# Kernel optimization log

Hardware: AMD Instinct MI355X
Metric: run time of the kernel (lower is better)

The kernel has to match this reference:

```python
import jax, jax.numpy as jnp
import numpy as np

N_NODES = 1000
N_EDGES = 8000
IN_FEATS = 64
HID = 128
RDIM = HID // 2  # UniversalReadout output dim
EPS = 1e-5


def _lrelu(v):
    return jax.nn.leaky_relu(v, 0.01)


def setup_inputs() -> dict:
    key = jax.random.key(0)
    ks = jax.random.split(key, 16)
    B = 128
    node_feats = jax.random.normal(ks[0], (B * N_NODES, IN_FEATS), jnp.float32)
    edge_weights = jax.random.uniform(ks[1], (B * N_EDGES,), jnp.float32)
    g_weights = jax.random.uniform(ks[2], (B * N_NODES,), jnp.float32)
    src = jax.random.randint(ks[3], (N_EDGES,), 0, N_NODES)
    dst = jax.random.randint(ks[4], (N_EDGES,), 0, N_NODES)
    # GraphConv weights (in, out), kaiming-ish scale
    W1 = jax.random.normal(ks[5], (IN_FEATS, HID), jnp.float32) / np.sqrt(IN_FEATS)
    W2 = jax.random.normal(ks[6], (HID, HID), jnp.float32) / np.sqrt(HID)
    W3 = jax.random.normal(ks[7], (HID, HID), jnp.float32) / np.sqrt(HID)
    suppl = jnp.ones((3, N_EDGES), jnp.float32)           # suppl_weights_conv1..3
    AR = jnp.ones((4, N_NODES), jnp.float32)              # AR1..AR4 weights
    gn_gamma = jnp.ones((3, HID), jnp.float32)
    gn_beta = jnp.zeros((3, HID), jnp.float32)
    gn_alpha = jnp.ones((3, HID), jnp.float32)            # GraphNorm mean-scale
    phi_W = jax.random.normal(ks[8], (3, HID, HID), jnp.float32) / np.sqrt(HID)
    phi_b = jnp.zeros((3, HID), jnp.float32)
    rho_W = jax.random.normal(ks[9], (3, HID, RDIM), jnp.float32) / np.sqrt(HID)
    rho_b = jnp.zeros((3, RDIM), jnp.float32)
    return dict(node_feats=node_feats, edge_weights=edge_weights, g_weights=g_weights,
                W1=W1, W2=W2, W3=W3, suppl=suppl, AR=AR,
                gn_gamma=gn_gamma, gn_beta=gn_beta, gn_alpha=gn_alpha,
                phi_W=phi_W, phi_b=phi_b, rho_W=rho_W, rho_b=rho_b,
                src=src, dst=dst)


def _forward(node_feats, edge_weights, g_weights, W1, W2, W3, suppl, AR,
             gn_gamma, gn_beta, gn_alpha, phi_W, phi_b, rho_W, rho_b, src, dst):
    B = node_feats.shape[0] // N_NODES
    x = node_feats.reshape(B, N_NODES, -1)        # (B, N, F)
    gw = g_weights.reshape(B, N_NODES)            # (B, N)
    ew = edge_weights.reshape(B, N_EDGES)         # (B, E)

    # structural degree normalization (norm='both'), shared topology
    deg_out = jnp.maximum(jnp.zeros((N_NODES,), x.dtype).at[src].add(1.0), 1.0)
    deg_in = jnp.maximum(jnp.zeros((N_NODES,), x.dtype).at[dst].add(1.0), 1.0)
    n_out = deg_out ** -0.5
    n_in = deg_in ** -0.5

    def gconv(h, W, ew_l):
        hs = h * n_out[None, :, None]
        msgs = hs[:, src, :] * ew_l[:, :, None]                       # (B, E, D)
        agg = jnp.zeros_like(hs).at[:, dst].add(msgs)                  # scatter-add
        return (agg * n_in[None, :, None]) @ W

    def gnorm(h, i):
        mean = h.mean(axis=1, keepdims=True)
        sub = h - gn_alpha[i] * mean
        var = (sub * sub).mean(axis=1, keepdims=True)
        return gn_gamma[i] * sub * jax.lax.rsqrt(var + EPS) + gn_beta[i]

    def uro(h, i):  # UniversalReadout (deep-sets): per-node MLP -> sum -> MLP
        z = _lrelu(h @ phi_W[i] + phi_b[i]).sum(axis=1)
        return _lrelu(z @ rho_W[i] + rho_b[i])

    def wmean(h, ar):  # dgl.mean_nodes with node weight: mean over nodes of w*x
        w = gw * ar[None, :]
        return (w[:, :, None] * h).mean(axis=1)

    pieces = [wmean(x, AR[0])]
    h = x
    Ws = (W1, W2, W3)
    for i in range(3):
        h = _lrelu(gnorm(gconv(h, Ws[i], ew * suppl[i][None, :]), i))
        pieces.append(uro(h, i))
        pieces.append(wmean(h, AR[i + 1]))
    return _lrelu(jnp.concatenate(pieces, axis=-1))


def reference(node_feats, edge_weights, g_weights, W1, W2, W3, suppl, AR,
              gn_gamma, gn_beta, gn_alpha, phi_W, phi_b, rho_W, rho_b, src, dst):
    return _forward(node_feats, edge_weights, g_weights, W1, W2, W3, suppl, AR,
                    gn_gamma, gn_beta, gn_alpha, phi_W, phi_b, rho_W, rho_b, src, dst)
```

## Files before the change

### kernel.cpp

```cpp
#include <hip/hip_runtime.h>
#include <cstddef>

#define NN 1000
#define NE 8000
#define FIN 64
#define DH 128
#define RD 64
#define FEPS 1e-5f

typedef short short8 __attribute__((ext_vector_type(8)));
typedef float f32x4 __attribute__((ext_vector_type(4)));

__device__ __forceinline__ float lrelu(float x){ return x > 0.f ? x : 0.01f*x; }

__device__ __forceinline__ unsigned short f2b(float x){
  union { float f; unsigned int u; } v; v.f = x;
  unsigned int r = (v.u + 0x7fffu + ((v.u >> 16) & 1u)) >> 16;
  return (unsigned short)r;
}
__device__ __forceinline__ float b2f(unsigned int lo16){
  union { unsigned int u; float f; } v; v.u = lo16 << 16; return v.f;
}
__device__ __forceinline__ unsigned int pack2(float a, float b){
  return (unsigned int)f2b(a) | ((unsigned int)f2b(b) << 16);
}


__global__ __launch_bounds__(1024) void k_topo(const int* __restrict__ src,
                       const int* __restrict__ dst,
                       float* nout, float* nin, int* rp,
                       int* csr_s, int* csr_e, int* csr_d){
  __shared__ int sdo[1024], sdi[1024], ssc[1024], sfill[1024];
  int t = threadIdx.x;
  sdo[t] = 0; sdi[t] = 0;
  __syncthreads();
  for (int e = t; e < NE; e += 1024){
    atomicAdd(&sdo[src[e]], 1);
    atomicAdd(&sdi[dst[e]], 1);
  }
  __syncthreads();
  int d = sdi[t];
  ssc[t] = d; __syncthreads();
  for (int off = 1; off < 1024; off <<= 1){
    int v = (t >= off) ? ssc[t-off] : 0;
    __syncthreads();
    ssc[t] += v;
    __syncthreads();
  }
  int myrp = ssc[t] - d;
  if (t < NN){
    rp[t] = myrp;
    nin[t]  = rsqrtf((float)max(sdi[t], 1));
    nout[t] = rsqrtf((float)max(sdo[t], 1));
  }
  if (t == NN-1) rp[NN] = ssc[t];
  sfill[t] = myrp;
  __syncthreads();
  for (int e = t; e < NE; e += 1024){
    int dn = dst[e];
    int pos = atomicAdd(&sfill[dn], 1);
    csr_s[pos] = src[e];
    csr_e[pos] = e;
    csr_d[pos] = dn;
  }
}


__global__ __launch_bounds__(256) void k_edge(const float* __restrict__ ew,
        const float* __restrict__ sup, const float* __restrict__ nout,
        const float* __restrict__ nin, const int* __restrict__ csr_s,
        const int* __restrict__ csr_e, const int* __restrict__ csr_d,
        int2* __restrict__ ecl, int B){
  int bid = blockIdx.x, t = threadIdx.x;
  int layer, b, q;
  if ((B & 7) == 0){
    int xcd = bid & 7, r = bid >> 3;
    int bsub = r/12, rem = r - bsub*12;
    layer = rem >> 2; q = rem & 3; b = bsub*8 + xcd;
  } else {
    layer = bid/(4*B);
    int rem = bid - layer*4*B;
    b = rem >> 2; q = rem & 3;
  }
  const float* ewb  = ew  + (size_t)b*NE;
  const float* supl = sup + (size_t)layer*NE;
  int2* o = ecl + ((size_t)layer*B + b)*NE;
  for (int k = q*2000 + t; k < q*2000 + 2000; k += 256){
    int e = csr_e[k]; int s = csr_s[k];
    float wv = ewb[e]*supl[e]*nout[s]*nin[csr_d[k]];
    int2 v; v.x = s; v.y = __float_as_int(wv);
    o[k] = v;
  }
}


__global__ __launch_bounds__(256) void k_misc(
        const float* __restrict__ W1, const float* __restrict__ W2,
        const float* __restrict__ W3, const float* __restrict__ phiW,
        unsigned short* __restrict__ wt,
        const float* __restrict__ x, unsigned short* __restrict__ xbf,
        const float* __restrict__ gw, const float* __restrict__ AR,
        float* __restrict__ out, int B){
  __shared__ float red[4][64];
  int bid = blockIdx.x, t = threadIdx.x;
  if (bid < 352){
    int i = bid*256 + t;
    if (i < 8192){
      int n = i >> 6, k = i & 63;
      wt[i] = f2b(W1[k*128 + n]);
    } else if (i < 24576){
      int j = i - 8192; int n = j >> 7, k = j & 127;
      wt[i] = f2b(W2[k*128 + n]);
    } else if (i < 40960){
      int j = i - 24576; int n = j >> 7, k = j & 127;
      wt[i] = f2b(W3[k*128 + n]);
    } else if (i < 90112){
      int j = i - 40960; int m = j >> 14; int jj = j & 16383;
      int n = jj >> 7, k = jj & 127;
      wt[i] = f2b(phiW[m*16384 + k*128 + n]);
    }
  } else {
    int wb = bid - 352;
    int b, q;
    if ((B & 7) == 0){
      int xcd = wb & 7, r = wb >> 3;
      int bsub = r >> 2; q = r & 3; b = bsub*8 + xcd;
    } else { b = wb >> 2; q = wb & 3; }
    int r = t >> 6, l = t & 63;
    float acc = 0.f;
    int v0 = q*250;
    for (int v = v0 + r; v < v0 + 250; v += 4){
      size_t idx = ((size_t)b*NN + v)*FIN + l;
      float xv = x[idx];
      xbf[idx] = f2b(xv);
      acc += gw[(size_t)b*NN + v]*AR[v]*xv;
    }
    red[r][l] = acc;
    __syncthreads();
    if (t < 64){
      float s = red[0][t]+red[1][t]+red[2][t]+red[3][t];
      atomicAdd(&out[(size_t)b*640 + t], s*(1.f/NN));
    }
  }
}


__global__ __launch_bounds__(256) void k_gathF(const unsigned short* __restrict__ xbf,
        const int2* __restrict__ ec, const int* __restrict__ rp,
        unsigned short* __restrict__ agg, int B){
  int bid = blockIdx.x;
  int b, chunk;
  if ((B & 7) == 0){
    int xcd = bid & 7, r = bid >> 3;
    int bsub = r/63; chunk = r - bsub*63; b = bsub*8 + xcd;
  } else { b = bid/63; chunk = bid - b*63; }
  int t = threadIdx.x;
  int grp = t >> 4, j = t & 15;
  int v = chunk*16 + grp; if (v >= NN) v = NN-1;
  int kb = rp[v], ke = rp[v+1];
  const unsigned short* xb = xbf + (size_t)b*NN*FIN;
  const int2* ecb = ec + (size_t)b*NE;
  float acc[4][4] = {};
  int k = kb;
  for (; k+3 < ke; k += 4){
    #pragma unroll
    for (int uu = 0; uu < 4; ++uu){
      int2 e = ecb[k+uu];
      uint2 u = *(const uint2*)(xb + e.x*FIN + j*4);
      float wgt = __int_as_float(e.y);
      acc[uu][0] = fmaf(b2f(u.x & 0xffffu), wgt, acc[uu][0]);
      acc[uu][1] = fmaf(b2f(u.x >> 16),     wgt, acc[uu][1]);
      acc[uu][2] = fmaf(b2f(u.y & 0xffffu), wgt, acc[uu][2]);
      acc[uu][3] = fmaf(b2f(u.y >> 16),     wgt, acc[uu][3]);
    }
  }
  for (; k < ke; ++k){
    int2 e = ecb[k];
    uint2 u = *(const uint2*)(xb + e.x*FIN + j*4);
    float wgt = __int_as_float(e.y);
    acc[0][0] = fmaf(b2f(u.x & 0xffffu), wgt, acc[0][0]);
    acc[0][1] = fmaf(b2f(u.x >> 16),     wgt, acc[0][1]);
    acc[0][2] = fmaf(b2f(u.y & 0xffffu), wgt, acc[0][2]);
    acc[0][3] = fmaf(b2f(u.y >> 16),     wgt, acc[0][3]);
  }
  uint2 o;
  o.x = pack2(acc[0][0]+acc[1][0]+acc[2][0]+acc[3][0],
              acc[0][1]+acc[1][1]+acc[2][1]+acc[3][1]);
  o.y = pack2(acc[0][2]+acc[1][2]+acc[2][2]+acc[3][2],
              acc[0][3]+acc[1][3]+acc[2][3]+acc[3][3]);
  *(uint2*)(agg + ((size_t)b*NN + v)*FIN + j*4) = o;
}


__global__ __launch_bounds__(256) void k_gathB(const unsigned short* __restrict__ h,
        const int2* __restrict__ ec, const int* __restrict__ rp,
        unsigned short* __restrict__ agg, int B){
  int bid = blockIdx.x;
  int b, chunk;
  if ((B & 7) == 0){
    int xcd = bid & 7, r = bid >> 3;
    int bsub = r/63; chunk = r - bsub*63; b = bsub*8 + xcd;
  } else { b = bid/63; chunk = bid - b*63; }
  int t = threadIdx.x;
  int grp = t >> 4, j = t & 15;
  int v = chunk*16 + grp; if (v >= NN) v = NN-1;
  int kb = rp[v], ke = rp[v+1];
  const unsigned short* hb = h + (size_t)b*NN*DH;
  const int2* ecb = ec + (size_t)b*NE;
  float acc[4][8] = {};
  int k = kb;
  for (; k+3 < ke; k += 4){
    #pragma unroll
    for (int uu = 0; uu < 4; ++uu){
      int2 e = ecb[k+uu];
      uint4 u = *(const uint4*)(hb + e.x*DH + j*8);
      float wgt = __int_as_float(e.y);
      acc[uu][0] = fmaf(b2f(u.x & 0xffffu), wgt, acc[uu][0]);
      acc[uu][1] = fmaf(b2f(u.x >> 16),     wgt, acc[uu][1]);
      acc[uu][2] = fmaf(b2f(u.y & 0xffffu), wgt, acc[uu][2]);
      acc[uu][3] = fmaf(b2f(u.y >> 16),     wgt, acc[uu][3]);
      acc[uu][4] = fmaf(b2f(u.z & 0xffffu), wgt, acc[uu][4]);
      acc[uu][5] = fmaf(b2f(u.z >> 16),     wgt, acc[uu][5]);
      acc[uu][6] = fmaf(b2f(u.w & 0xffffu), wgt, acc[uu][6]);
      acc[uu][7] = fmaf(b2f(u.w >> 16),     wgt, acc[uu][7]);
    }
  }
  for (; k < ke; ++k){
    int2 e = ecb[k];
    uint4 u = *(const uint4*)(hb + e.x*DH + j*8);
    float wgt = __int_as_float(e.y);
    acc[0][0] = fmaf(b2f(u.x & 0xffffu), wgt, acc[0][0]);
    acc[0][1] = fmaf(b2f(u.x >> 16),     wgt, acc[0][1]);
    acc[0][2] = fmaf(b2f(u.y & 0xffffu), wgt, acc[0][2]);
    acc[0][3] = fmaf(b2f(u.y >> 16),     wgt, acc[0][3]);
    acc[0][4] = fmaf(b2f(u.z & 0xffffu), wgt, acc[0][4]);
    acc[0][5] = fmaf(b2f(u.z >> 16),     wgt, acc[0][5]);
    acc[0][6] = fmaf(b2f(u.w & 0xffffu), wgt, acc[0][6]);
    acc[0][7] = fmaf(b2f(u.w >> 16),     wgt, acc[0][7]);
  }
  float f[8];
  #pragma unroll
  for (int d2 = 0; d2 < 8; ++d2)
    f[d2] = acc[0][d2]+acc[1][d2]+acc[2][d2]+acc[3][d2];
  uint4 o;
  o.x = pack2(f[0],f[1]); o.y = pack2(f[2],f[3]);
  o.z = pack2(f[4],f[5]); o.w = pack2(f[6],f[7]);
  *(uint4*)(agg + ((size_t)b*NN + v)*DH + j*8) = o;
}


template<int K>
__global__ __launch_bounds__(256) void k_conv(const unsigned short* __restrict__ A,
        const unsigned short* __restrict__ Wt, unsigned short* __restrict__ Cb,
        float* __restrict__ red_out, int B){
  constexpr int K2 = K*2;
  constexpr int CPR = K/8;
  __shared__ __align__(16) char smem[64*K2 + 128*K2];
  char* sA = smem;
  char* sW = smem + 64*K2;
  int t = threadIdx.x;
  int b, tile;
  if ((B & 7) == 0){
    int xcd = blockIdx.x & 7, r = blockIdx.x >> 3;
    int bsub = r >> 4; tile = r & 15; b = bsub*8 + xcd;
  } else { b = blockIdx.x >> 4; tile = blockIdx.x & 15; }
  int rows = NN - tile*64; if (rows > 64) rows = 64;
  size_t row0 = (size_t)b*NN + tile*64;
  size_t Mtot = (size_t)B*NN;

  for (int i = t; i < 64*CPR; i += 256){
    int r = i/CPR, cb = i%CPR;
    size_t gr = row0 + r; if (gr >= Mtot) gr = Mtot - 1;
    uint4 v = *(const uint4*)(A + gr*K + cb*8);
    *(uint4*)(sA + r*K2 + ((cb*16) ^ ((r & 7) << 4))) = v;
  }
  for (int i = t; i < 128*CPR; i += 256){
    int n = i/CPR, cb = i%CPR;
    uint4 v = *(const uint4*)(Wt + n*K + cb*8);
    *(uint4*)(sW + n*K2 + ((cb*16) ^ ((n & 7) << 4))) = v;
  }
  __syncthreads();

  int w = t >> 6, l = t & 63;
  int lr = l & 15, lk = l >> 4;
  f32x4 acc[8] = {};
  int arow = w*16 + lr;
  #pragma unroll
  for (int kk = 0; kk < K/32; ++kk){
    int kb = kk*64 + lk*16;
    short8 a = *(const short8*)(sA + arow*K2 + (kb ^ ((arow & 7) << 4)));
    #pragma unroll
    for (int f = 0; f < 8; ++f){
      int n = f*16 + lr;
      short8 bf = *(const short8*)(sW + n*K2 + (kb ^ ((n & 7) << 4)));
      acc[f] = __builtin_amdgcn_mfma_f32_16x16x32_bf16(a, bf, acc[f], 0, 0, 0);
    }
  }
  __syncthreads();

  float* red = (float*)smem;
  float cs[8], cq[8];
  int rbase = w*16 + lk*4;
  #pragma unroll
  for (int f = 0; f < 8; ++f){
    int col = f*16 + lr;
    float s = 0.f, q = 0.f;
    #pragma unroll
    for (int r = 0; r < 4; ++r){
      int row = rbase + r;
      bool ok = row < rows;
      float v = acc[f][r];
      if (ok) Cb[(row0 + row)*DH + col] = f2b(v);
      s += ok ? v : 0.f;
      q += ok ? v*v : 0.f;
    }
    s += __shfl_xor(s, 16); s += __shfl_xor(s, 32);
    q += __shfl_xor(q, 16); q += __shfl_xor(q, 32);
    cs[f] = s; cq[f] = q;
  }
  if (l < 16){
    #pragma unroll
    for (int f = 0; f < 8; ++f){
      red[w*128 + f*16 + l] = cs[f];
      red[512 + w*128 + f*16 + l] = cq[f];
    }
  }
  __syncthreads();
  if (t < 128){
    float s = red[t] + red[128+t] + red[256+t] + red[384+t];
    atomicAdd(&red_out[(size_t)b*DH + t], s);
    float q = red[512+t] + red[640+t] + red[768+t] + red[896+t];
    atomicAdd(&red_out[(size_t)B*DH + (size_t)b*DH + t], q);
  }
}


__global__ __launch_bounds__(256) void k_phi(const unsigned short* __restrict__ hpre,
        const unsigned short* __restrict__ Wt,
        const float* __restrict__ ssum, const float* __restrict__ ssq,
        const float* __restrict__ alpha, const float* __restrict__ gamma,
        const float* __restrict__ beta, const float* __restrict__ bias,
        const float* __restrict__ gw, const float* __restrict__ ar,
        unsigned short* __restrict__ hnorm,
        float* __restrict__ zout, float* __restrict__ out, int off, int B){
  __shared__ __align__(16) char smem[64*256 + 128*256];
  __shared__ __align__(16) float sivg[128], spc[128];
  __shared__ float sgw[64];
  char* sA = smem;
  char* sW = smem + 64*256;
  int t = threadIdx.x;
  int b, tile;
  if ((B & 7) == 0){
    int xcd = blockIdx.x & 7, r = blockIdx.x >> 3;
    int bsub = r >> 4; tile = r & 15; b = bsub*8 + xcd;
  } else { b = blockIdx.x >> 4; tile = blockIdx.x & 15; }
  int rows = NN - tile*64; if (rows > 64) rows = 64;
  size_t row0 = (size_t)b*NN + tile*64;

  if (t < 128){
    float m   = ssum[(size_t)b*DH + t]*(1.f/NN);
    float ex2 = ssq [(size_t)b*DH + t]*(1.f/NN);
    float a = alpha[t];
    float var = ex2 - (2.f*a - a*a)*m*m;
    float g = gamma[t]*rsqrtf(var + FEPS);
    sivg[t] = g;
    spc [t] = beta[t] - a*m*g;
  } else if (t < 192){
    int vr = tile*64 + (t - 128);
    sgw[t-128] = (vr < NN) ? gw[(size_t)b*NN + vr]*ar[vr] : 0.f;
  }
  __syncthreads();

  for (int i = t; i < 64*16; i += 256){
    int r = i >> 4, cb = i & 15;
    int rr = (r < rows) ? r : 0;
    uint4 u = *(const uint4*)(hpre + (row0 + rr)*DH + cb*8);
    int c0 = cb*8;
    float4 g1 = *(const float4*)(sivg + c0), g2 = *(const float4*)(sivg + c0 + 4);
    float4 p1 = *(const float4*)(spc + c0),  p2 = *(const float4*)(spc + c0 + 4);
    float xv[8];
    xv[0] = b2f(u.x & 0xffffu); xv[1] = b2f(u.x >> 16);
    xv[2] = b2f(u.y & 0xffffu); xv[3] = b2f(u.y >> 16);
    xv[4] = b2f(u.z & 0xffffu); xv[5] = b2f(u.z >> 16);
    xv[6] = b2f(u.w & 0xffffu); xv[7] = b2f(u.w >> 16);
    float gg[8] = {g1.x,g1.y,g1.z,g1.w,g2.x,g2.y,g2.z,g2.w};
    float pv[8] = {p1.x,p1.y,p1.z,p1.w,p2.x,p2.y,p2.z,p2.w};
    float nv[8];
    #pragma unroll
    for (int d2 = 0; d2 < 8; ++d2){
      float n0 = fmaf(xv[d2], gg[d2], pv[d2]);
      nv[d2] = fmaxf(n0, 0.01f*n0);
    }
    uint4 o;
    o.x = pack2(nv[0],nv[1]); o.y = pack2(nv[2],nv[3]);
    o.z = pack2(nv[4],nv[5]); o.w = pack2(nv[6],nv[7]);
    *(uint4*)(sA + r*256 + ((cb*16) ^ ((r & 7) << 4))) = o;
    if (r < rows) *(uint4*)(hnorm + (row0 + r)*DH + cb*8) = o;
  }
  for (int i = t; i < 128*16; i += 256){
    int n = i >> 4, cb = i & 15;
    uint4 v = *(const uint4*)(Wt + n*DH + cb*8);
    *(uint4*)(sW + n*256 + ((cb*16) ^ ((n & 7) << 4))) = v;
  }
  __syncthreads();

  int w = t >> 6, l = t & 63;
  int lr = l & 15, lk = l >> 4;
  f32x4 acc[8] = {};
  int arow = w*16 + lr;
  #pragma unroll
  for (int kk = 0; kk < 4; ++kk){
    int kb = kk*64 + lk*16;
    short8 a = *(const short8*)(sA + arow*256 + (kb ^ ((arow & 7) << 4)));
    #pragma unroll
    for (int f = 0; f < 8; ++f){
      int n = f*16 + lr;
      short8 bf = *(const short8*)(sW + n*256 + (kb ^ ((n & 7) << 4)));
      acc[f] = __builtin_amdgcn_mfma_f32_16x16x32_bf16(a, bf, acc[f], 0, 0, 0);
    }
  }
  __syncthreads();

  float* red = (float*)sW;
  float cs[8];
  int rbase = w*16 + lk*4;
  #pragma unroll
  for (int f = 0; f < 8; ++f){
    int col = f*16 + lr;
    float bv = bias[col];
    float s = 0.f;
    #pragma unroll
    for (int r = 0; r < 4; ++r){
      int row = rbase + r;
      float u = lrelu(acc[f][r] + bv);
      s += (row < rows) ? u : 0.f;
    }
    s += __shfl_xor(s, 16); s += __shfl_xor(s, 32);
    cs[f] = s;
  }
  if (l < 16){
    #pragma unroll
    for (int f = 0; f < 8; ++f) red[w*128 + f*16 + l] = cs[f];
  }
  __syncthreads();
  if (t < 128){
    float s = red[t] + red[128+t] + red[256+t] + red[384+t];
    atomicAdd(&zout[(size_t)b*DH + t], s);
  } else {
    int col = t - 128;
    float s = 0.f;
    for (int r = 0; r < 64; ++r){
      int byteoff = r*256 + (((col >> 3)*16) ^ ((r & 7) << 4)) + (col & 7)*2;
      s += sgw[r]*b2f(*(const unsigned short*)(sA + byteoff));
    }
    atomicAdd(&out[(size_t)b*640 + off + col], s*(1.f/NN));
  }
}


__global__ void k_rho(const float* __restrict__ statz, const float* __restrict__ rhoW,
                      const float* __restrict__ rhob, float* __restrict__ out, int B){
  int i = blockIdx.x / B, b = blockIdx.x % B;
  int d = threadIdx.x;
  const float* z = statz + (size_t)i*3*B*DH + (size_t)2*B*DH + (size_t)b*DH;
  float acc = rhob[i*RD + d];
  const float* Wm = rhoW + (size_t)i*DH*RD;
  for (int k = 0; k < DH; ++k) acc = fmaf(z[k], Wm[k*RD + d], acc);
  out[(size_t)b*640 + 64 + i*192 + d] = lrelu(acc);
}

__global__ void k_flrelu(float* o, int n){
  int i = blockIdx.x*blockDim.x + threadIdx.x;
  if (i < n) o[i] = lrelu(o[i]);
}


extern "C" void kernel_launch(void* const* d_in, const int* in_sizes, int n_in,
                              void* d_out, int out_size, void* d_ws, size_t ws_size,
                              hipStream_t stream){
  const float* x    = (const float*)d_in[0];
  const float* ew   = (const float*)d_in[1];
  const float* gw   = (const float*)d_in[2];
  const float* W1   = (const float*)d_in[3];
  const float* W2   = (const float*)d_in[4];
  const float* W3   = (const float*)d_in[5];
  const float* sup  = (const float*)d_in[6];
  const float* AR   = (const float*)d_in[7];
  const float* gam  = (const float*)d_in[8];
  const float* bet  = (const float*)d_in[9];
  const float* alp  = (const float*)d_in[10];
  const float* phiW = (const float*)d_in[11];
  const float* phib = (const float*)d_in[12];
  const float* rhoW = (const float*)d_in[13];
  const float* rhob = (const float*)d_in[14];
  const int*   src  = (const int*)d_in[15];
  const int*   dst  = (const int*)d_in[16];
  float* out = (float*)d_out;

  int B = in_sizes[0] / (NN*FIN);
  size_t M = (size_t)B*NN;
  size_t BD = (size_t)B*DH;

  float* w = (float*)d_ws;
  size_t p = 0;
  float* nout = w+p; p += 1024;
  float* nin  = w+p; p += 1024;
  int* rp     = (int*)(w+p); p += 1024;
  int* csr_s  = (int*)(w+p); p += 8192;
  int* csr_e  = (int*)(w+p); p += 8192;
  int* csr_d  = (int*)(w+p); p += 8192;
  float* statz = w+p; p += 3*3*BD;
  unsigned short* wt = (unsigned short*)(w+p); p += 45056;
  int2* ecl   = (int2*)(w+p); p += (size_t)6*B*NE;
  unsigned short* xbf   = (unsigned short*)(w+p); p += M*FIN/2;
  unsigned short* hpre  = (unsigned short*)(w+p); p += M*DH/2;
  unsigned short* hnorm = (unsigned short*)(w+p); p += M*DH/2;
  unsigned short* agg   = (unsigned short*)(w+p); p += M*DH/2;

  hipMemsetAsync(out, 0, (size_t)out_size*sizeof(float), stream);
  hipMemsetAsync(statz, 0, 9*BD*sizeof(float), stream);

  k_topo<<<1, 1024, 0, stream>>>(src, dst, nout, nin, rp, csr_s, csr_e, csr_d);
  k_edge<<<12*B, 256, 0, stream>>>(ew, sup, nout, nin, csr_s, csr_e, csr_d, ecl, B);
  k_misc<<<352 + B*4, 256, 0, stream>>>(W1, W2, W3, phiW, wt, x, xbf, gw, AR, out, B);

  const int wt_off[3] = {0, 8192, 24576};

  for (int i = 0; i < 3; ++i){
    float* SS = statz + (size_t)i*3*BD;
    if (i == 0){
      k_gathF<<<B*63, 256, 0, stream>>>(xbf, ecl, rp, agg, B);
      k_conv<FIN><<<B*16, 256, 0, stream>>>(agg, wt, hpre, SS, B);
    } else {
      k_gathB<<<B*63, 256, 0, stream>>>(hnorm, ecl + (size_t)i*B*NE, rp, agg, B);
      k_conv<DH><<<B*16, 256, 0, stream>>>(agg, wt + wt_off[i], hpre, SS, B);
    }
    k_phi<<<B*16, 256, 0, stream>>>(hpre, wt + 40960 + i*16384,
        SS, SS + BD, alp + i*DH, gam + i*DH, bet + i*DH, phib + i*DH,
        gw, AR + (size_t)(i+1)*NN, hnorm, SS + 2*BD, out, 128 + i*192, B);
  }

  k_rho<<<3*B, RD, 0, stream>>>(statz, rhoW, rhob, out, B);
  k_flrelu<<<(B*640+255)/256, 256, 0, stream>>>(out, B*640);
}
```

Before: 308.5 us.

## Merge prep kernels, sort nodes by degree, gather fp32 input directly

Topology construction, weight conversion and the input weighted mean are folded into one prep kernel. The prep kernel also builds a degree-sorted node order, which the gather kernels use to balance the work within each block. The first-layer gather now reads the fp32 input directly, so the bf16 copy of x is no longer made. Other changes remove launches and traffic: the statz memset moves into k_edge, rho and the final leaky-relu are fused into one kernel, and the last layer skips writing hnorm. The trade-offs are more fp32 bytes read in the first gather and a prep kernel that runs serially on one block.

```diff
diff --git a/kernel.cpp b/kernel.cpp
--- a/kernel.cpp
+++ b/kernel.cpp
@@ -26,42 +26,100 @@
 }
 
 
-__global__ __launch_bounds__(1024) void k_topo(const int* __restrict__ src,
-                       const int* __restrict__ dst,
-                       float* nout, float* nin, int* rp,
-                       int* csr_s, int* csr_e, int* csr_d){
+__global__ __launch_bounds__(1024) void k_prep(const int* __restrict__ src,
+        const int* __restrict__ dst,
+        const float* __restrict__ W1, const float* __restrict__ W2,
+        const float* __restrict__ W3, const float* __restrict__ phiW,
+        unsigned short* __restrict__ wt,
+        const float* __restrict__ x, const float* __restrict__ gw,
+        const float* __restrict__ AR, float* __restrict__ out,
+        float* nout, float* nin, int* rp, int* ord,
+        int* csr_s, int* csr_e, int* csr_d, int B){
   __shared__ int sdo[1024], sdi[1024], ssc[1024], sfill[1024];
-  int t = threadIdx.x;
-  sdo[t] = 0; sdi[t] = 0;
-  __syncthreads();
-  for (int e = t; e < NE; e += 1024){
-    atomicAdd(&sdo[src[e]], 1);
-    atomicAdd(&sdi[dst[e]], 1);
-  }
-  __syncthreads();
-  int d = sdi[t];
-  ssc[t] = d; __syncthreads();
-  for (int off = 1; off < 1024; off <<= 1){
-    int v = (t >= off) ? ssc[t-off] : 0;
-    __syncthreads();
-    ssc[t] += v;
-    __syncthreads();
-  }
-  int myrp = ssc[t] - d;
-  if (t < NN){
-    rp[t] = myrp;
-    nin[t]  = rsqrtf((float)max(sdi[t], 1));
-    nout[t] = rsqrtf((float)max(sdo[t], 1));
-  }
-  if (t == NN-1) rp[NN] = ssc[t];
-  sfill[t] = myrp;
-  __syncthreads();
-  for (int e = t; e < NE; e += 1024){
-    int dn = dst[e];
-    int pos = atomicAdd(&sfill[dn], 1);
-    csr_s[pos] = src[e];
-    csr_e[pos] = e;
-    csr_d[pos] = dn;
+  __shared__ int hist[256], hoff[256];
+  __shared__ float red2[16][64];
+  int bid = blockIdx.x, t = threadIdx.x;
+
+  if (bid == 0){
+    sdo[t] = 0; sdi[t] = 0;
+    __syncthreads();
+    for (int e = t; e < NE; e += 1024){
+      atomicAdd(&sdo[src[e]], 1);
+      atomicAdd(&sdi[dst[e]], 1);
+    }
+    __syncthreads();
+    int d = sdi[t];
+    ssc[t] = d; __syncthreads();
+    for (int off = 1; off < 1024; off <<= 1){
+      int v = (t >= off) ? ssc[t-off] : 0;
+      __syncthreads();
+      ssc[t] += v;
+      __syncthreads();
+    }
+    int myrp = ssc[t] - d;
+    if (t < NN){
+      rp[t] = myrp;
+      nin[t]  = rsqrtf((float)max(sdi[t], 1));
+      nout[t] = rsqrtf((float)max(sdo[t], 1));
+    }
+    if (t == NN-1) rp[NN] = ssc[t];
+    sfill[t] = myrp;
+    __syncthreads();
+    for (int e = t; e < NE; e += 1024){
+      int dn = dst[e];
+      int pos = atomicAdd(&sfill[dn], 1);
+      csr_s[pos] = src[e];
+      csr_e[pos] = e;
+      csr_d[pos] = dn;
+    }
+    if (t < 256) hist[t] = 0;
+    __syncthreads();
+    if (t < NN) atomicAdd(&hist[min(sdi[t], 255)], 1);
+    __syncthreads();
+    if (t < 256) hoff[t] = hist[t];
+    __syncthreads();
+    for (int off = 1; off < 256; off <<= 1){
+      int v = (t < 256 && t >= off) ? hoff[t-off] : 0;
+      __syncthreads();
+      if (t < 256) hoff[t] += v;
+      __syncthreads();
+    }
+    if (t < 256) hoff[t] -= hist[t];
+    __syncthreads();
+    if (t < NN){
+      int pos = atomicAdd(&hoff[min(sdi[t], 255)], 1);
+      ord[pos] = t;
+    }
+  } else if (bid <= 88){
+    int i = (bid-1)*1024 + t;
+    if (i < 8192){
+      int n = i >> 6, k = i & 63;
+      wt[i] = f2b(W1[k*128 + n]);
+    } else if (i < 24576){
+      int j = i - 8192; int n = j >> 7, k = j & 127;
+      wt[i] = f2b(W2[k*128 + n]);
+    } else if (i < 40960){
+      int j = i - 24576; int n = j >> 7, k = j & 127;
+      wt[i] = f2b(W3[k*128 + n]);
+    } else {
+      int j = i - 40960; int m = j >> 14; int jj = j & 16383;
+      int n = jj >> 7, k = jj & 127;
+      wt[i] = f2b(phiW[m*16384 + k*128 + n]);
+    }
+  } else {
+    int b = bid - 89;
+    int r = t >> 6, l = t & 63;
+    float acc = 0.f;
+    for (int v = r; v < NN; v += 16)
+      acc += gw[(size_t)b*NN + v]*AR[v]*x[((size_t)b*NN + v)*FIN + l];
+    red2[r][l] = acc;
+    __syncthreads();
+    if (t < 64){
+      float s = 0.f;
+      #pragma unroll
+      for (int g2 = 0; g2 < 16; ++g2) s += red2[g2][t];
+      out[(size_t)b*640 + t] = s*(1.f/NN);
+    }
   }
 }
 
@@ -70,8 +128,10 @@
         const float* __restrict__ sup, const float* __restrict__ nout,
         const float* __restrict__ nin, const int* __restrict__ csr_s,
         const int* __restrict__ csr_e, const int* __restrict__ csr_d,
-        int2* __restrict__ ecl, int B){
+        int2* __restrict__ ecl, float* __restrict__ statz, int nz4, int B){
   int bid = blockIdx.x, t = threadIdx.x;
+  int gi = bid*256 + t;
+  if (gi < nz4) ((float4*)statz)[gi] = make_float4(0.f,0.f,0.f,0.f);
   int layer, b, q;
   if ((B & 7) == 0){
     int xcd = bid & 7, r = bid >> 3;
@@ -94,60 +154,9 @@
 }
 
 
-__global__ __launch_bounds__(256) void k_misc(
-        const float* __restrict__ W1, const float* __restrict__ W2,
-        const float* __restrict__ W3, const float* __restrict__ phiW,
-        unsigned short* __restrict__ wt,
-        const float* __restrict__ x, unsigned short* __restrict__ xbf,
-        const float* __restrict__ gw, const float* __restrict__ AR,
-        float* __restrict__ out, int B){
-  __shared__ float red[4][64];
-  int bid = blockIdx.x, t = threadIdx.x;
-  if (bid < 352){
-    int i = bid*256 + t;
-    if (i < 8192){
-      int n = i >> 6, k = i & 63;
-      wt[i] = f2b(W1[k*128 + n]);
-    } else if (i < 24576){
-      int j = i - 8192; int n = j >> 7, k = j & 127;
-      wt[i] = f2b(W2[k*128 + n]);
-    } else if (i < 40960){
-      int j = i - 24576; int n = j >> 7, k = j & 127;
-      wt[i] = f2b(W3[k*128 + n]);
-    } else if (i < 90112){
-      int j = i - 40960; int m = j >> 14; int jj = j & 16383;
-      int n = jj >> 7, k = jj & 127;
-      wt[i] = f2b(phiW[m*16384 + k*128 + n]);
-    }
-  } else {
-    int wb = bid - 352;
-    int b, q;
-    if ((B & 7) == 0){
-      int xcd = wb & 7, r = wb >> 3;
-      int bsub = r >> 2; q = r & 3; b = bsub*8 + xcd;
-    } else { b = wb >> 2; q = wb & 3; }
-    int r = t >> 6, l = t & 63;
-    float acc = 0.f;
-    int v0 = q*250;
-    for (int v = v0 + r; v < v0 + 250; v += 4){
-      size_t idx = ((size_t)b*NN + v)*FIN + l;
-      float xv = x[idx];
-      xbf[idx] = f2b(xv);
-      acc += gw[(size_t)b*NN + v]*AR[v]*xv;
-    }
-    red[r][l] = acc;
-    __syncthreads();
-    if (t < 64){
-      float s = red[0][t]+red[1][t]+red[2][t]+red[3][t];
-      atomicAdd(&out[(size_t)b*640 + t], s*(1.f/NN));
-    }
-  }
-}
-
-
-__global__ __launch_bounds__(256) void k_gathF(const unsigned short* __restrict__ xbf,
+__global__ __launch_bounds__(256) void k_gathF(const float* __restrict__ x,
         const int2* __restrict__ ec, const int* __restrict__ rp,
-        unsigned short* __restrict__ agg, int B){
+        const int* __restrict__ ord, unsigned short* __restrict__ agg, int B){
   int bid = blockIdx.x;
   int b, chunk;
   if ((B & 7) == 0){
@@ -156,9 +165,10 @@
   } else { b = bid/63; chunk = bid - b*63; }
   int t = threadIdx.x;
   int grp = t >> 4, j = t & 15;
-  int v = chunk*16 + grp; if (v >= NN) v = NN-1;
+  int rk = chunk*16 + grp; if (rk > NN-1) rk = NN-1;
+  int v = ord[rk];
   int kb = rp[v], ke = rp[v+1];
-  const unsigned short* xb = xbf + (size_t)b*NN*FIN;
+  const float* xb = x + (size_t)b*NN*FIN;
   const int2* ecb = ec + (size_t)b*NE;
   float acc[4][4] = {};
   int k = kb;
@@ -166,22 +176,22 @@
     #pragma unroll
     for (int uu = 0; uu < 4; ++uu){
       int2 e = ecb[k+uu];
-      uint2 u = *(const uint2*)(xb + e.x*FIN + j*4);
+      float4 xr = *(const float4*)(xb + e.x*FIN + j*4);
       float wgt = __int_as_float(e.y);
-      acc[uu][0] = fmaf(b2f(u.x & 0xffffu), wgt, acc[uu][0]);
-      acc[uu][1] = fmaf(b2f(u.x >> 16),     wgt, acc[uu][1]);
-      acc[uu][2] = fmaf(b2f(u.y & 0xffffu), wgt, acc[uu][2]);
-      acc[uu][3] = fmaf(b2f(u.y >> 16),     wgt, acc[uu][3]);
+      acc[uu][0] = fmaf(xr.x, wgt, acc[uu][0]);
+      acc[uu][1] = fmaf(xr.y, wgt, acc[uu][1]);
+      acc[uu][2] = fmaf(xr.z, wgt, acc[uu][2]);
+      acc[uu][3] = fmaf(xr.w, wgt, acc[uu][3]);
     }
   }
   for (; k < ke; ++k){
     int2 e = ecb[k];
-    uint2 u = *(const uint2*)(xb + e.x*FIN + j*4);
+    float4 xr = *(const float4*)(xb + e.x*FIN + j*4);
     float wgt = __int_as_float(e.y);
-    acc[0][0] = fmaf(b2f(u.x & 0xffffu), wgt, acc[0][0]);
-    acc[0][1] = fmaf(b2f(u.x >> 16),     wgt, acc[0][1]);
-    acc[0][2] = fmaf(b2f(u.y & 0xffffu), wgt, acc[0][2]);
-    acc[0][3] = fmaf(b2f(u.y >> 16),     wgt, acc[0][3]);
+    acc[0][0] = fmaf(xr.x, wgt, acc[0][0]);
+    acc[0][1] = fmaf(xr.y, wgt, acc[0][1]);
+    acc[0][2] = fmaf(xr.z, wgt, acc[0][2]);
+    acc[0][3] = fmaf(xr.w, wgt, acc[0][3]);
   }
   uint2 o;
   o.x = pack2(acc[0][0]+acc[1][0]+acc[2][0]+acc[3][0],
@@ -194,7 +204,7 @@
 
 __global__ __launch_bounds__(256) void k_gathB(const unsigned short* __restrict__ h,
         const int2* __restrict__ ec, const int* __restrict__ rp,
-        unsigned short* __restrict__ agg, int B){
+        const int* __restrict__ ord, unsigned short* __restrict__ agg, int B){
   int bid = blockIdx.x;
   int b, chunk;
   if ((B & 7) == 0){
@@ -203,7 +213,8 @@
   } else { b = bid/63; chunk = bid - b*63; }
   int t = threadIdx.x;
   int grp = t >> 4, j = t & 15;
-  int v = chunk*16 + grp; if (v >= NN) v = NN-1;
+  int rk = chunk*16 + grp; if (rk > NN-1) rk = NN-1;
+  int v = ord[rk];
   int kb = rp[v], ke = rp[v+1];
   const unsigned short* hb = h + (size_t)b*NN*DH;
   const int2* ecb = ec + (size_t)b*NE;
@@ -395,7 +406,8 @@
     o.x = pack2(nv[0],nv[1]); o.y = pack2(nv[2],nv[3]);
     o.z = pack2(nv[4],nv[5]); o.w = pack2(nv[6],nv[7]);
     *(uint4*)(sA + r*256 + ((cb*16) ^ ((r & 7) << 4))) = o;
-    if (r < rows) *(uint4*)(hnorm + (row0 + r)*DH + cb*8) = o;
+    if (hnorm != nullptr && r < rows)
+      *(uint4*)(hnorm + (row0 + r)*DH + cb*8) = o;
   }
   for (int i = t; i < 128*16; i += 256){
     int n = i >> 4, cb = i & 15;
@@ -458,20 +470,25 @@
 }
 
 
-__global__ void k_rho(const float* __restrict__ statz, const float* __restrict__ rhoW,
-                      const float* __restrict__ rhob, float* __restrict__ out, int B){
-  int i = blockIdx.x / B, b = blockIdx.x % B;
-  int d = threadIdx.x;
-  const float* z = statz + (size_t)i*3*B*DH + (size_t)2*B*DH + (size_t)b*DH;
-  float acc = rhob[i*RD + d];
-  const float* Wm = rhoW + (size_t)i*DH*RD;
-  for (int k = 0; k < DH; ++k) acc = fmaf(z[k], Wm[k*RD + d], acc);
-  out[(size_t)b*640 + 64 + i*192 + d] = lrelu(acc);
-}
-
-__global__ void k_flrelu(float* o, int n){
-  int i = blockIdx.x*blockDim.x + threadIdx.x;
-  if (i < n) o[i] = lrelu(o[i]);
+__global__ void k_final(const float* __restrict__ statz, const float* __restrict__ rhoW,
+                        const float* __restrict__ rhob, float* __restrict__ out, int B){
+  int b = blockIdx.x;
+  int t = threadIdx.x;
+  if (t < 192){
+    int i = t >> 6, d = t & 63;
+    const float* z = statz + ((size_t)i*3 + 2)*(size_t)B*DH + (size_t)b*DH;
+    float acc = rhob[i*RD + d];
+    const float* Wm = rhoW + (size_t)i*DH*RD;
+    for (int k = 0; k < DH; ++k) acc = fmaf(z[k], Wm[k*RD + d], acc);
+    out[(size_t)b*640 + 64 + i*192 + d] = lrelu(lrelu(acc));
+  }
+  for (int s = t; s < 448; s += 256){
+    int idx;
+    if (s < 64) idx = s;
+    else { int j = s - 64; idx = 128 + (j >> 7)*192 + (j & 127); }
+    size_t gi = (size_t)b*640 + idx;
+    out[gi] = lrelu(out[gi]);
+  }
 }
 
 
@@ -506,40 +523,40 @@
   float* nout = w+p; p += 1024;
   float* nin  = w+p; p += 1024;
   int* rp     = (int*)(w+p); p += 1024;
+  int* ord    = (int*)(w+p); p += 1024;
   int* csr_s  = (int*)(w+p); p += 8192;
   int* csr_e  = (int*)(w+p); p += 8192;
   int* csr_d  = (int*)(w+p); p += 8192;
   float* statz = w+p; p += 3*3*BD;
   unsigned short* wt = (unsigned short*)(w+p); p += 45056;
   int2* ecl   = (int2*)(w+p); p += (size_t)6*B*NE;
-  unsigned short* xbf   = (unsigned short*)(w+p); p += M*FIN/2;
   unsigned short* hpre  = (unsigned short*)(w+p); p += M*DH/2;
   unsigned short* hnorm = (unsigned short*)(w+p); p += M*DH/2;
   unsigned short* agg   = (unsigned short*)(w+p); p += M*DH/2;
 
   hipMemsetAsync(out, 0, (size_t)out_size*sizeof(float), stream);
-  hipMemsetAsync(statz, 0, 9*BD*sizeof(float), stream);
-
-  k_topo<<<1, 1024, 0, stream>>>(src, dst, nout, nin, rp, csr_s, csr_e, csr_d);
-  k_edge<<<12*B, 256, 0, stream>>>(ew, sup, nout, nin, csr_s, csr_e, csr_d, ecl, B);
-  k_misc<<<352 + B*4, 256, 0, stream>>>(W1, W2, W3, phiW, wt, x, xbf, gw, AR, out, B);
+
+  k_prep<<<89 + B, 1024, 0, stream>>>(src, dst, W1, W2, W3, phiW, wt,
+      x, gw, AR, out, nout, nin, rp, ord, csr_s, csr_e, csr_d, B);
+  k_edge<<<12*B, 256, 0, stream>>>(ew, sup, nout, nin, csr_s, csr_e, csr_d,
+      ecl, statz, (int)(9*BD/4), B);
 
   const int wt_off[3] = {0, 8192, 24576};
 
   for (int i = 0; i < 3; ++i){
     float* SS = statz + (size_t)i*3*BD;
     if (i == 0){
-      k_gathF<<<B*63, 256, 0, stream>>>(xbf, ecl, rp, agg, B);
+      k_gathF<<<B*63, 256, 0, stream>>>(x, ecl, rp, ord, agg, B);
       k_conv<FIN><<<B*16, 256, 0, stream>>>(agg, wt, hpre, SS, B);
     } else {
-      k_gathB<<<B*63, 256, 0, stream>>>(hnorm, ecl + (size_t)i*B*NE, rp, agg, B);
+      k_gathB<<<B*63, 256, 0, stream>>>(hnorm, ecl + (size_t)i*B*NE, rp, ord, agg, B);
       k_conv<DH><<<B*16, 256, 0, stream>>>(agg, wt + wt_off[i], hpre, SS, B);
     }
     k_phi<<<B*16, 256, 0, stream>>>(hpre, wt + 40960 + i*16384,
         SS, SS + BD, alp + i*DH, gam + i*DH, bet + i*DH, phib + i*DH,
-        gw, AR + (size_t)(i+1)*NN, hnorm, SS + 2*BD, out, 128 + i*192, B);
-  }
-
-  k_rho<<<3*B, RD, 0, stream>>>(statz, rhoW, rhob, out, B);
-  k_flrelu<<<(B*640+255)/256, 256, 0, stream>>>(out, B*640);
-}
+        gw, AR + (size_t)(i+1)*NN, (i == 2) ? nullptr : hnorm,
+        SS + 2*BD, out, 128 + i*192, B);
+  }
+
+  k_final<<<B, 256, 0, stream>>>(statz, rhoW, rhob, out, B);
+}
```

Result: faster. 268.5 us (median of 3 runs) (-13.0%).
